# Kernel tuning notes

Measured on AMD Instinct MI355X. Metric: run time of the kernel, lower is better.

## Reference

```python
import jax, jax.numpy as jnp
import numpy as np

B, T, H, S, P, NH, NL = 16, 4096, 1024, 16, 6, 8, 2
EPS = 1e-5

def _ln(x, g, b):
    m = x.mean(-1, keepdims=True)
    v = ((x - m) ** 2).mean(-1, keepdims=True)
    return (x - m) / jnp.sqrt(v + EPS) * g + b

def _mha(q, k, v, in_w, in_b, out_w, out_b, kpm):
    dh = H // NH
    wq, wk, wv = jnp.split(in_w, 3, axis=0)
    bq, bk, bv = jnp.split(in_b, 3, axis=0)
    qh = (q @ wq.T + bq).reshape(q.shape[0], q.shape[1], NH, dh)
    kh = (k @ wk.T + bk).reshape(k.shape[0], k.shape[1], NH, dh)
    vh = (v @ wv.T + bv).reshape(v.shape[0], v.shape[1], NH, dh)
    sc = jnp.einsum('bqhd,bkhd->bhqk', qh, kh) / np.float32(np.sqrt(dh))
    if kpm is not None:
        sc = jnp.where(kpm[:, None, None, :], -1e30, sc)
    a = jax.nn.softmax(sc, axis=-1)
    o = jnp.einsum('bhqk,bkhd->bqhd', a, vh).reshape(q.shape[0], q.shape[1], H)
    return o @ out_w.T + out_b

def _segment_pool(hidden, mask):
    # vectorized ragged per-segment mean over the valid prefix of each sequence
    L = mask.sum(-1)  # [B] valid lengths (assumed >= S)
    s = jnp.arange(S + 1, dtype=jnp.float32)
    bounds = jnp.floor(s[None, :] * L[:, None].astype(jnp.float32) / S).astype(jnp.int32)  # [B,S+1]
    pos = jnp.arange(T)
    valid = pos[None, :] < L[:, None]  # [B,T]
    seg_id = (pos[None, :, None] >= bounds[:, None, 1:S]).sum(-1)  # [B,T] in [0,S-1]
    oh = ((seg_id[:, :, None] == jnp.arange(S)) & valid[:, :, None]).astype(hidden.dtype)  # [B,T,S]
    seg_sum = jnp.einsum('bts,bth->bsh', oh, hidden)
    cnt = oh.sum(1)  # [B,S]
    seg_states = seg_sum / jnp.maximum(cnt, 1.0)[..., None]
    return seg_states, cnt > 0

def setup_inputs() -> dict:
    key = jax.random.key(0)
    ks = jax.random.split(key, 32)
    p = lambda k, shp: (jax.random.normal(k, shp, jnp.float32) * 0.02)
    token_states = jax.random.normal(ks[0], (B, T, H), jnp.float32)
    lengths = jax.random.randint(ks[1], (B,), T // 2, T + 1)
    attention_mask = (jnp.arange(T)[None, :] < lengths[:, None]).astype(jnp.int32)
    inp = dict(
        token_states=token_states, attention_mask=attention_mask,
        sa_in_w=p(ks[2], (3 * H, H)), sa_in_b=jnp.zeros((3 * H,)),
        sa_out_w=p(ks[3], (H, H)), sa_out_b=jnp.zeros((H,)),
        ln_g=jnp.ones((H,)), ln_b=jnp.zeros((H,)),
        sal_w1=p(ks[4], (H, H)), sal_b1=jnp.zeros((H,)),
        sal_w2=p(ks[5], (1, H)), sal_b2=jnp.zeros((1,)),
        plan_q=p(ks[6], (P, H)),
        qa_in_w=p(ks[7], (3 * H, H)), qa_in_b=jnp.zeros((3 * H,)),
        qa_out_w=p(ks[8], (H, H)), qa_out_b=jnp.zeros((H,)),
        r_in_w=p(ks[9], (NL, 3 * H, H)), r_in_b=jnp.zeros((NL, 3 * H)),
        r_out_w=p(ks[10], (NL, H, H)), r_out_b=jnp.zeros((NL, H)),
        r_ln1_g=jnp.ones((NL, H)), r_ln1_b=jnp.zeros((NL, H)),
        r_ln2_g=jnp.ones((NL, H)), r_ln2_b=jnp.zeros((NL, H)),
        r_w1=p(ks[11], (NL, 4 * H, H)), r_b1=jnp.zeros((NL, 4 * H)),
        r_w2=p(ks[12], (NL, H, 4 * H)), r_b2=jnp.zeros((NL, H)),
    )
    return inp

def reference(token_states, attention_mask, sa_in_w, sa_in_b, sa_out_w, sa_out_b,
              ln_g, ln_b, sal_w1, sal_b1, sal_w2, sal_b2, plan_q,
              qa_in_w, qa_in_b, qa_out_w, qa_out_b,
              r_in_w, r_in_b, r_out_w, r_out_b,
              r_ln1_g, r_ln1_b, r_ln2_g, r_ln2_b, r_w1, r_b1, r_w2, r_b2):
    seg, seg_mask = _segment_pool(token_states, attention_mask)
    kpm = ~seg_mask
    attn = _mha(seg, seg, seg, sa_in_w, sa_in_b, sa_out_w, sa_out_b, kpm)
    seg = _ln(seg + attn, ln_g, ln_b)
    h = jax.nn.gelu(seg @ sal_w1.T + sal_b1, approximate=False)
    logits = (h @ sal_w2.T + sal_b2)[..., 0]
    logits = jnp.where(seg_mask, logits, -10000.0)
    sal = jax.nn.softmax(logits, axis=-1)
    wseg = seg * sal[..., None]
    query = jnp.broadcast_to(plan_q[None], (token_states.shape[0], P, H))
    plan = _mha(query, wseg, wseg, qa_in_w, qa_in_b, qa_out_w, qa_out_b, kpm)
    for l in range(NL):  # norm_first TransformerEncoder layers
        y = _ln(plan, r_ln1_g[l], r_ln1_b[l])
        plan = plan + _mha(y, y, y, r_in_w[l], r_in_b[l], r_out_w[l], r_out_b[l], None)
        y = _ln(plan, r_ln2_g[l], r_ln2_b[l])
        y = jax.nn.gelu(y @ r_w1[l].T + r_b1[l], approximate=False) @ r_w2[l].T + r_b2[l]
        plan = plan + y
    entropy = -(sal * jnp.log(sal + 1e-8)).sum(-1).mean()
    nrm = jnp.maximum(jnp.linalg.norm(plan, axis=-1, keepdims=True), 1e-12)
    npn = plan / nrm
    sim = jnp.einsum('bph,bqh->bpq', npn, npn)
    off = sim * (1.0 - jnp.eye(P, dtype=sim.dtype))
    redundancy = (off ** 2).sum() / (plan.shape[0] * P * (P - 1))
    return plan, sal, entropy, redundancy
```

## Files before the change

### kernel.cpp

```cpp
#include <hip/hip_runtime.h>
#include <hip/hip_bf16.h>
#include <math.h>

#define BB 16
#define TT 4096
#define HH 1024
#define SS 16
#define PP 6
#define NHH 8
#define DHH 128
#define NLL 2

typedef __hip_bfloat16 bf16;

__device__ __forceinline__ float b2f(bf16 x){ return __bfloat162float(x); }
__device__ __forceinline__ float us2f(unsigned short u){ return __uint_as_float(((unsigned)u) << 16); }

template<int ISBF>
__device__ __forceinline__ float ldw(const void* p, size_t i){
    if (ISBF) return b2f(((const bf16*)p)[i]);
    else      return ((const float*)p)[i];
}

__global__ void k_len(const int* __restrict__ mask, int* __restrict__ L,
                      const unsigned* __restrict__ lng, float* __restrict__ scal,
                      int* __restrict__ flag){
    int b = blockIdx.x, tid = threadIdx.x;
    if (b == 0 && tid == 0){
        scal[0] = 0.f; scal[1] = 0.f; scal[2] = 0.f; scal[3] = 0.f;
        flag[0] = (lng[0] == 0x3F800000u) ? 0 : 1;
    }
    int s = 0;
    for (int t = tid; t < TT; t += 256) s += mask[b*TT + t];
    __shared__ int red[256];
    red[tid] = s; __syncthreads();
    for (int w = 128; w > 0; w >>= 1){ if (tid < w) red[tid] += red[tid+w]; __syncthreads(); }
    if (tid == 0) L[b] = red[0];
}

template<int ISBF>
__device__ void segpool_body(const void* __restrict__ tok, const int* __restrict__ L,
                             float* __restrict__ seg){
    __shared__ float sm[8*1024];
    int s = blockIdx.x, b = blockIdx.y, tid = threadIdx.x;
    int len = L[b];
    int lo = (s*len)/SS, hi = ((s+1)*len)/SS;
    float inv = 1.0f/(float)(hi-lo);
    if (ISBF){
        int ro = tid >> 7;
        int c8 = (tid & 127) << 3;
        float a[8];
        #pragma unroll
        for (int i = 0; i < 8; ++i) a[i] = 0.f;
        const unsigned short* t = (const unsigned short*)tok;
        for (int tt = lo + ro; tt < hi; tt += 8){
            uint4 u = *(const uint4*)(t + ((size_t)(b*TT + tt))*HH + c8);
            a[0] += us2f((unsigned short)(u.x & 0xffff)); a[1] += us2f((unsigned short)(u.x >> 16));
            a[2] += us2f((unsigned short)(u.y & 0xffff)); a[3] += us2f((unsigned short)(u.y >> 16));
            a[4] += us2f((unsigned short)(u.z & 0xffff)); a[5] += us2f((unsigned short)(u.z >> 16));
            a[6] += us2f((unsigned short)(u.w & 0xffff)); a[7] += us2f((unsigned short)(u.w >> 16));
        }
        #pragma unroll
        for (int i = 0; i < 8; ++i) sm[ro*1024 + c8 + i] = a[i];
        __syncthreads();
        if (ro == 0){
            #pragma unroll
            for (int r = 1; r < 8; ++r)
                #pragma unroll
                for (int i = 0; i < 8; ++i) a[i] += sm[r*1024 + c8 + i];
            float* o = seg + ((size_t)(b*SS + s))*HH + c8;
            #pragma unroll
            for (int i = 0; i < 8; ++i) o[i] = a[i]*inv;
        }
    } else {
        int ro = tid >> 8;
        int c4 = (tid & 255) << 2;
        float a[4] = {0.f,0.f,0.f,0.f};
        const float* t = (const float*)tok;
        for (int tt = lo + ro; tt < hi; tt += 4){
            float4 u = *(const float4*)(t + ((size_t)(b*TT + tt))*HH + c4);
            a[0] += u.x; a[1] += u.y; a[2] += u.z; a[3] += u.w;
        }
        #pragma unroll
        for (int i = 0; i < 4; ++i) sm[ro*1024 + c4 + i] = a[i];
        __syncthreads();
        if (ro == 0){
            #pragma unroll
            for (int r = 1; r < 4; ++r)
                #pragma unroll
                for (int i = 0; i < 4; ++i) a[i] += sm[r*1024 + c4 + i];
            float* o = seg + ((size_t)(b*SS + s))*HH + c4;
            #pragma unroll
            for (int i = 0; i < 4; ++i) o[i] = a[i]*inv;
        }
    }
}
__global__ __launch_bounds__(1024) void k_segpool(const void* __restrict__ tok,
                          const int* __restrict__ L,
                          float* __restrict__ seg, const int* __restrict__ flag){
    if (*flag) segpool_body<1>(tok, L, seg); else segpool_body<0>(tok, L, seg);
}

__global__ __launch_bounds__(256,2) void k_gemmsk(
        const float* __restrict__ X, const void* __restrict__ W,
        float* __restrict__ part, int N, int K, int M,
        size_t offW, int kChunk, const int* __restrict__ flag){
    __shared__ float As[16][68], Bs[16][68];
    const int tid = threadIdx.x;
    const int r0 = blockIdx.y*64, c0 = blockIdx.x*64;
    const int tx = tid & 15, ty = tid >> 4;
    const int sr = tid >> 2;
    const int sk = (tid & 3) << 2;
    const int kbeg = blockIdx.z * kChunk, kend = kbeg + kChunk;
    const int isbf = *flag;
    float c[4][4] = {{0.f,0.f,0.f,0.f},{0.f,0.f,0.f,0.f},{0.f,0.f,0.f,0.f},{0.f,0.f,0.f,0.f}};
    for (int k0 = kbeg; k0 < kend; k0 += 16){
        float4 av = make_float4(0.f,0.f,0.f,0.f);
        if (r0 + sr < N) av = *(const float4*)(X + (size_t)(r0+sr)*K + k0 + sk);
        float4 bv;
        if (isbf){
            ushort4 u = *(const ushort4*)((const bf16*)W + offW + (size_t)(c0+sr)*K + k0 + sk);
            bv = make_float4(us2f(u.x), us2f(u.y), us2f(u.z), us2f(u.w));
        } else {
            bv = *(const float4*)((const float*)W + offW + (size_t)(c0+sr)*K + k0 + sk);
        }
        As[sk+0][sr]=av.x; As[sk+1][sr]=av.y; As[sk+2][sr]=av.z; As[sk+3][sr]=av.w;
        Bs[sk+0][sr]=bv.x; Bs[sk+1][sr]=bv.y; Bs[sk+2][sr]=bv.z; Bs[sk+3][sr]=bv.w;
        __syncthreads();
        #pragma unroll
        for (int kk = 0; kk < 16; ++kk){
            float4 a = *(const float4*)&As[kk][ty<<2];
            float4 b = *(const float4*)&Bs[kk][tx<<2];
            c[0][0] += a.x*b.x; c[0][1] += a.x*b.y; c[0][2] += a.x*b.z; c[0][3] += a.x*b.w;
            c[1][0] += a.y*b.x; c[1][1] += a.y*b.y; c[1][2] += a.y*b.z; c[1][3] += a.y*b.w;
            c[2][0] += a.z*b.x; c[2][1] += a.z*b.y; c[2][2] += a.z*b.z; c[2][3] += a.z*b.w;
            c[3][0] += a.w*b.x; c[3][1] += a.w*b.y; c[3][2] += a.w*b.z; c[3][3] += a.w*b.w;
        }
        __syncthreads();
    }
    float* dst = part + (size_t)blockIdx.z * ((size_t)N * M);
    #pragma unroll
    for (int i = 0; i < 4; ++i){
        int r = r0 + (ty<<2) + i;
        if (r < N){
            float4 st = make_float4(c[i][0], c[i][1], c[i][2], c[i][3]);
            *(float4*)(dst + (size_t)r*M + c0 + (tx<<2)) = st;
        }
    }
}

template<int ACT, int RES>
__global__ void k_epi(const float* __restrict__ part, const void* __restrict__ bias,
                      const float* __restrict__ R, float* __restrict__ Y,
                      int M, int offB, int total, int SK, const int* __restrict__ flag){
    int i = blockIdx.x*256 + threadIdx.x;
    if (i >= total) return;
    float v = 0.f;
    for (int z = 0; z < SK; ++z) v += part[(size_t)z*total + i];
    int col = i % M;
    v += (*flag) ? b2f(((const bf16*)bias)[offB + col]) : ((const float*)bias)[offB + col];
    if (ACT == 1) v = 0.5f*v*(1.0f + erff(v*0.70710678118654752f));
    if (RES == 1) v += R[i];
    Y[i] = v;
}

template<int ISBF, int RES>
__device__ void epiln_body(const float* __restrict__ part, const void* __restrict__ bias,
                           const float* __restrict__ R, float* __restrict__ Y,
                           float* __restrict__ Z, const void* __restrict__ g,
                           const void* __restrict__ bta,
                           int offB, int lnoff, int N, int SK){
    int row = blockIdx.x, tid = threadIdx.x;
    size_t base = (size_t)row*HH;
    size_t total = (size_t)N*HH;
    float v[4]; float s = 0.f, sq = 0.f;
    #pragma unroll
    for (int u = 0; u < 4; ++u){
        int c = tid + u*256;
        float a = 0.f;
        for (int z = 0; z < SK; ++z) a += part[(size_t)z*total + base + c];
        a += ldw<ISBF>(bias, (size_t)(offB + c));
        if (RES) a += R[base + c];
        Y[base + c] = a;
        v[u] = a; s += a; sq += a*a;
    }
    __shared__ float r1[256], r2[256];
    r1[tid] = s; r2[tid] = sq; __syncthreads();
    for (int w = 128; w > 0; w >>= 1){
        if (tid < w){ r1[tid] += r1[tid+w]; r2[tid] += r2[tid+w]; }
        __syncthreads();
    }
    float mean = r1[0]*(1.0f/HH);
    float var  = fmaxf(r2[0]*(1.0f/HH) - mean*mean, 0.f);
    float rstd = rsqrtf(var + 1e-5f);
    #pragma unroll
    for (int u = 0; u < 4; ++u){
        int c = tid + u*256;
        Z[base + c] = (v[u]-mean)*rstd*ldw<ISBF>(g, (size_t)(lnoff+c)) + ldw<ISBF>(bta, (size_t)(lnoff+c));
    }
}
template<int RES>
__global__ void k_epiln(const float* __restrict__ part, const void* __restrict__ bias,
                        const float* __restrict__ R, float* __restrict__ Y,
                        float* __restrict__ Z, const void* __restrict__ g,
                        const void* __restrict__ bta, int offB, int lnoff, int N, int SK,
                        const int* __restrict__ flag){
    if (*flag) epiln_body<1,RES>(part,bias,R,Y,Z,g,bta,offB,lnoff,N,SK);
    else       epiln_body<0,RES>(part,bias,R,Y,Z,g,bta,offB,lnoff,N,SK);
}

static void gemm_sk(hipStream_t st, const float* X, const void* W, const void* bias,
                    const float* R, float* Y, float* part, const int* flag,
                    int N, int K, int M, size_t offW, int offB, int SK, int act, int res){
    dim3 g(M/64, (N+63)/64, SK);
    k_gemmsk<<<g, 256, 0, st>>>(X, W, part, N, K, M, offW, K/SK, flag);
    int total = N*M;
    int nb = (total + 255)/256;
    if (act){
        if (res) k_epi<1,1><<<nb,256,0,st>>>(part, bias, R, Y, M, offB, total, SK, flag);
        else     k_epi<1,0><<<nb,256,0,st>>>(part, bias, R, Y, M, offB, total, SK, flag);
    } else {
        if (res) k_epi<0,1><<<nb,256,0,st>>>(part, bias, R, Y, M, offB, total, SK, flag);
        else     k_epi<0,0><<<nb,256,0,st>>>(part, bias, R, Y, M, offB, total, SK, flag);
    }
}

static void gemm_skln(hipStream_t st, const float* X, const void* W, const void* bias,
                      const float* R, float* Y, float* Z, const void* g, const void* bta,
                      float* part, const int* flag,
                      int N, int K, int M, size_t offW, int offB, int lnoff, int SK, int res){
    dim3 gr(M/64, (N+63)/64, SK);
    k_gemmsk<<<gr, 256, 0, st>>>(X, W, part, N, K, M, offW, K/SK, flag);
    if (res) k_epiln<1><<<N,256,0,st>>>(part, bias, R, Y, Z, g, bta, offB, lnoff, N, SK, flag);
    else     k_epiln<0><<<N,256,0,st>>>(part, bias, R, Y, Z, g, bta, offB, lnoff, N, SK, flag);
}

__global__ void k_attn(const float* __restrict__ Qb, const float* __restrict__ Kb,
                       const float* __restrict__ Vb, float* __restrict__ O,
                       int nq, int nk, int sQ, int sKV, int qShared){
    __shared__ float Qs[16][132], Ks[16][132], Vs[16][132];
    __shared__ float sc[16][17];
    int b = blockIdx.x / NHH, h = blockIdx.x % NHH;
    int tid = threadIdx.x;
    for (int idx = tid; idx < nq*32; idx += 256){
        int i = idx >> 5, d4 = (idx & 31) << 2;
        int r = qShared ? i : (b*nq + i);
        *(float4*)&Qs[i][d4] = *(const float4*)&Qb[(size_t)r*sQ + h*DHH + d4];
    }
    for (int idx = tid; idx < nk*32; idx += 256){
        int j = idx >> 5, d4 = (idx & 31) << 2;
        *(float4*)&Ks[j][d4] = *(const float4*)&Kb[(size_t)(b*nk + j)*sKV + h*DHH + d4];
        *(float4*)&Vs[j][d4] = *(const float4*)&Vb[(size_t)(b*nk + j)*sKV + h*DHH + d4];
    }
    __syncthreads();
    const float scale = 0.0883883476483184406f;
    for (int idx = tid; idx < nq*nk; idx += 256){
        int i = idx / nk, j = idx - i*nk;
        const float4* qp = (const float4*)&Qs[i][0];
        const float4* kp = (const float4*)&Ks[j][0];
        float ax=0.f, ay=0.f, az=0.f, aw=0.f;
        #pragma unroll
        for (int k4 = 0; k4 < 32; ++k4){
            float4 a = qp[k4], c = kp[k4];
            ax += a.x*c.x; ay += a.y*c.y; az += a.z*c.z; aw += a.w*c.w;
        }
        sc[i][j] = (ax+ay+az+aw) * scale;
    }
    __syncthreads();
    if (tid < nq){
        float m = -1e30f;
        for (int j = 0; j < nk; ++j) m = fmaxf(m, sc[tid][j]);
        float ssum = 0.f;
        for (int j = 0; j < nk; ++j){ float e = expf(sc[tid][j] - m); sc[tid][j] = e; ssum += e; }
        float inv = 1.0f/ssum;
        for (int j = 0; j < nk; ++j) sc[tid][j] *= inv;
    }
    __syncthreads();
    for (int idx = tid; idx < nq*32; idx += 256){
        int i = idx >> 5, d4 = (idx & 31) << 2;
        float ox=0.f, oy=0.f, oz=0.f, ow=0.f;
        for (int j = 0; j < nk; ++j){
            float s = sc[i][j];
            float4 v = *(const float4*)&Vs[j][d4];
            ox += s*v.x; oy += s*v.y; oz += s*v.z; ow += s*v.w;
        }
        float4 o = make_float4(ox,oy,oz,ow);
        *(float4*)&O[(size_t)(b*nq + i)*HH + h*DHH + d4] = o;
    }
}

template<int ISBF>
__device__ void sallogit_body(const float* __restrict__ Hbuf, const void* __restrict__ w2,
                              const void* __restrict__ b2v, float* __restrict__ lg){
    int s = blockIdx.x, b = blockIdx.y, tid = threadIdx.x;
    const float* hr = Hbuf + (size_t)(b*SS + s)*HH;
    float acc = 0.f;
    #pragma unroll
    for (int u = 0; u < 4; ++u){ int c = tid + u*256; acc += hr[c]*ldw<ISBF>(w2, (size_t)c); }
    __shared__ float red[256];
    red[tid] = acc; __syncthreads();
    for (int w = 128; w > 0; w >>= 1){ if (tid < w) red[tid] += red[tid+w]; __syncthreads(); }
    if (tid == 0) lg[b*SS + s] = red[0] + ldw<ISBF>(b2v, 0);
}
__global__ void k_sallogit(const float* __restrict__ Hbuf, const void* __restrict__ w2,
                           const void* __restrict__ b2v, float* __restrict__ lg,
                           const int* __restrict__ flag){
    if (*flag) sallogit_body<1>(Hbuf,w2,b2v,lg); else sallogit_body<0>(Hbuf,w2,b2v,lg);
}
__global__ void k_salsm(const float* __restrict__ lg, float* __restrict__ sal,
                        float* __restrict__ scal){
    int b = blockIdx.x;
    if (threadIdx.x == 0){
        float e[SS];
        float m = -1e30f;
        for (int s = 0; s < SS; ++s) m = fmaxf(m, lg[b*SS+s]);
        float ssum = 0.f;
        for (int s = 0; s < SS; ++s){ e[s] = expf(lg[b*SS+s]-m); ssum += e[s]; }
        float inv = 1.0f/ssum, ent = 0.f;
        for (int s = 0; s < SS; ++s){
            float p = e[s]*inv;
            sal[b*SS+s] = p;
            ent -= p*logf(p + 1e-8f);
        }
        atomicAdd(&scal[0], ent);
    }
}

__global__ void k_wseg(const float* __restrict__ seg, const float* __restrict__ sal,
                       float* __restrict__ wseg){
    int i = blockIdx.x*256 + threadIdx.x;
    wseg[i] = seg[i]*sal[i/HH];
}

__global__ void k_cvt(const void* __restrict__ in, float* __restrict__ out, int n,
                      const int* __restrict__ flag){
    int i = blockIdx.x*256 + threadIdx.x;
    if (i < n){
        if (*flag) out[i] = b2f(((const bf16*)in)[i]);
        else       out[i] = ((const float*)in)[i];
    }
}

__device__ const int g_PR[21] = {0,1,2,3,4,5, 0,0,0,0,0,1,1,1,1,2,2,2,3,3,4};
__device__ const int g_QR[21] = {0,1,2,3,4,5, 1,2,3,4,5,2,3,4,5,3,4,5,4,5,5};

__global__ void k_dots(const float* __restrict__ plan, float* __restrict__ dots){
    int t = blockIdx.x % 21, b = blockIdx.x / 21, tid = threadIdx.x;
    const float* X = plan + (size_t)b*PP*HH + (size_t)g_PR[t]*HH;
    const float* Yv = plan + (size_t)b*PP*HH + (size_t)g_QR[t]*HH;
    float acc = 0.f;
    #pragma unroll
    for (int u = 0; u < 4; ++u){ int c = tid + u*256; acc += X[c]*Yv[c]; }
    __shared__ float red[256];
    red[tid] = acc; __syncthreads();
    for (int w = 128; w > 0; w >>= 1){ if (tid < w) red[tid] += red[tid+w]; __syncthreads(); }
    if (tid == 0) dots[b*24 + t] = red[0];
}
__global__ void k_red2(const float* __restrict__ dots, float* __restrict__ scal){
    __shared__ float tot[BB];
    int tid = threadIdx.x;
    if (tid < BB){
        float n[PP];
        #pragma unroll
        for (int p = 0; p < PP; ++p) n[p] = fmaxf(sqrtf(dots[tid*24 + p]), 1e-12f);
        float total = 0.f;
        for (int k = 6; k < 21; ++k){
            float s = dots[tid*24 + k] / (n[g_PR[k]]*n[g_QR[k]]);
            total += 2.0f*s*s;
        }
        tot[tid] = total;
    }
    __syncthreads();
    if (tid == 0){
        float s = 0.f;
        for (int i = 0; i < BB; ++i) s += tot[i];
        scal[1] = s;
    }
}

__global__ void k_out(const float* __restrict__ plan, const float* __restrict__ sal,
                      const float* __restrict__ scal, void* __restrict__ outv,
                      const int* __restrict__ flag){
    int i = blockIdx.x*256 + threadIdx.x;
    const int NPLAN = BB*PP*HH;
    const int NSAL  = BB*SS;
    float v;
    if (i < NPLAN) v = plan[i];
    else if (i < NPLAN + NSAL) v = sal[i - NPLAN];
    else if (i == NPLAN + NSAL) v = scal[0] * (1.0f/BB);
    else if (i == NPLAN + NSAL + 1) v = scal[1] * (1.0f/(BB*PP*(PP-1)));
    else return;
    if (*flag) ((bf16*)outv)[i] = __float2bfloat16(v);
    else       ((float*)outv)[i] = v;
}

extern "C" void kernel_launch(void* const* d_in, const int* in_sizes, int n_in,
                              void* d_out, int out_size, void* d_ws, size_t ws_size,
                              hipStream_t stream) {
    const void* tok      = d_in[0];
    const int*  mask     = (const int*)d_in[1];
    const void* sa_in_w  = d_in[2];
    const void* sa_in_b  = d_in[3];
    const void* sa_out_w = d_in[4];
    const void* sa_out_b = d_in[5];
    const void* ln_g     = d_in[6];
    const void* ln_b     = d_in[7];
    const void* sal_w1   = d_in[8];
    const void* sal_b1   = d_in[9];
    const void* sal_w2   = d_in[10];
    const void* sal_b2   = d_in[11];
    const void* plan_q   = d_in[12];
    const void* qa_in_w  = d_in[13];
    const void* qa_in_b  = d_in[14];
    const void* qa_out_w = d_in[15];
    const void* qa_out_b = d_in[16];
    const void* r_in_w   = d_in[17];
    const void* r_in_b   = d_in[18];
    const void* r_out_w  = d_in[19];
    const void* r_out_b  = d_in[20];
    const void* r_ln1_g  = d_in[21];
    const void* r_ln1_b  = d_in[22];
    const void* r_ln2_g  = d_in[23];
    const void* r_ln2_b  = d_in[24];
    const void* r_w1     = d_in[25];
    const void* r_b1     = d_in[26];
    const void* r_w2     = d_in[27];
    const void* r_b2     = d_in[28];

    float* ws   = (float*)d_ws;
    float* seg  = ws;
    float* qkv  = seg  + BB*SS*HH;
    float* t1   = qkv  + BB*SS*3*HH;
    float* t2   = t1   + BB*SS*HH;
    float* plan = t2   + BB*SS*HH;
    float* ybuf = plan + BB*PP*HH;
    float* qkv2 = ybuf + BB*PP*HH;
    float* pbuf = qkv2 + BB*PP*4*HH;
    float* sal  = pbuf + BB*PP*HH;
    float* qx   = sal  + BB*SS;
    float* qh   = qx   + PP*HH;
    float* lgbuf= qh   + PP*HH;
    float* dots = lgbuf+ BB*SS;
    float* part = dots + BB*24;
    float* scal = part + 4*BB*SS*3*HH;
    int*   Lw   = (int*)(scal + 4);
    int*   flag = Lw + BB;

    k_len<<<BB, 256, 0, stream>>>(mask, Lw, (const unsigned*)ln_g, scal, flag);
    k_segpool<<<dim3(SS, BB), 1024, 0, stream>>>(tok, Lw, seg, flag);

    gemm_sk(stream, seg, sa_in_w, sa_in_b, nullptr, qkv, part, flag,
            BB*SS, HH, 3*HH, (size_t)0, 0, 4, 0, 0);
    k_attn<<<BB*NHH, 256, 0, stream>>>(qkv, qkv+HH, qkv+2*HH, t1, SS, SS, 3*HH, 3*HH, 0);
    gemm_skln(stream, t1, sa_out_w, sa_out_b, seg, t2, seg, ln_g, ln_b, part, flag,
              BB*SS, HH, HH, (size_t)0, 0, 0, 8, 1);

    gemm_sk(stream, seg, sal_w1, sal_b1, nullptr, t1, part, flag,
            BB*SS, HH, HH, (size_t)0, 0, 8, 1, 0);
    k_sallogit<<<dim3(SS, BB), 256, 0, stream>>>(t1, sal_w2, sal_b2, lgbuf, flag);
    k_salsm<<<BB, 64, 0, stream>>>(lgbuf, sal, scal);
    k_wseg<<<BB*SS*HH/256, 256, 0, stream>>>(seg, sal, t2);

    k_cvt<<<(PP*HH+255)/256, 256, 0, stream>>>(plan_q, qx, PP*HH, flag);
    gemm_sk(stream, qx, qa_in_w, qa_in_b, nullptr, qh, part, flag,
            PP, HH, HH, (size_t)0, 0, 16, 0, 0);
    gemm_sk(stream, t2, qa_in_w, qa_in_b, nullptr, qkv, part, flag,
            BB*SS, HH, 2*HH, (size_t)HH*HH, HH, 4, 0, 0);
    k_attn<<<BB*NHH, 256, 0, stream>>>(qh, qkv, qkv+HH, pbuf, PP, SS, HH, 2*HH, 1);
    gemm_skln(stream, pbuf, qa_out_w, qa_out_b, nullptr, plan, ybuf, r_ln1_g, r_ln1_b,
              part, flag, BB*PP, HH, HH, (size_t)0, 0, 0, 8, 0);

    for (int l = 0; l < NLL; ++l){
        gemm_sk(stream, ybuf, r_in_w, r_in_b, nullptr, qkv2, part, flag,
                BB*PP, HH, 3*HH, (size_t)l*3*HH*HH, l*3*HH, 4, 0, 0);
        k_attn<<<BB*NHH, 256, 0, stream>>>(qkv2, qkv2+HH, qkv2+2*HH, pbuf, PP, PP, 3*HH, 3*HH, 0);
        gemm_skln(stream, pbuf, r_out_w, r_out_b, plan, plan, ybuf, r_ln2_g, r_ln2_b,
                  part, flag, BB*PP, HH, HH, (size_t)l*HH*HH, l*HH, l*HH, 8, 1);
        gemm_sk(stream, ybuf, r_w1, r_b1, nullptr, qkv2, part, flag,
                BB*PP, HH, 4*HH, (size_t)l*4*HH*HH, l*4*HH, 4, 1, 0);
        if (l < NLL-1){
            gemm_skln(stream, qkv2, r_w2, r_b2, plan, plan, ybuf, r_ln1_g, r_ln1_b,
                      part, flag, BB*PP, 4*HH, HH, (size_t)l*HH*4*HH, l*HH, (l+1)*HH, 16, 1);
        } else {
            gemm_sk(stream, qkv2, r_w2, r_b2, plan, plan, part, flag,
                    BB*PP, 4*HH, HH, (size_t)l*HH*4*HH, l*HH, 16, 0, 1);
        }
    }

    k_dots<<<BB*21, 256, 0, stream>>>(plan, dots);
    k_red2<<<1, 64, 0, stream>>>(dots, scal);
    k_out<<<(BB*PP*HH + BB*SS + 2 + 255)/256, 256, 0, stream>>>(plan, sal, scal, d_out, flag);
}
```

Measured before the change: 882.2 us.

## Use bf16 MFMA GEMM with hi/lo split activations for bf16 weights

Replaces the scalar FP32 LDS-tiled GEMM with a matrix-core path (16x16x32 bf16 MFMA) whenever the weights are bf16. Each activation is split into a bf16 high part and a bf16 residual so that FP32 activation precision is roughly kept. Producer kernels (segpool, epilogues, attention, wseg, cvt) now also write these hi/lo bf16 copies. Split-K factors are retuned as well. The cost is extra memory writes and two MFMAs per K step, plus loading weights directly from global memory with no LDS reuse across waves. The FP32-weight path keeps the old scalar GEMM and only gains the extra conversion stores.

```diff
diff --git a/kernel.cpp b/kernel.cpp
--- a/kernel.cpp
+++ b/kernel.cpp
@@ -12,9 +12,23 @@
 #define NLL 2
 
 typedef __hip_bfloat16 bf16;
+typedef __attribute__((ext_vector_type(8))) short s8v;
+typedef __attribute__((ext_vector_type(4))) float f32x4;
+
+#define MFMA_B16(a,b,c) __builtin_amdgcn_mfma_f32_16x16x32_bf16((a),(b),(c),0,0,0)
 
 __device__ __forceinline__ float b2f(bf16 x){ return __bfloat162float(x); }
 __device__ __forceinline__ float us2f(unsigned short u){ return __uint_as_float(((unsigned)u) << 16); }
+
+__device__ __forceinline__ void split_bf(float x, ushort& h, ushort& l){
+    unsigned xb = __float_as_uint(x);
+    unsigned hh = (xb + 0x7FFFu + ((xb >> 16) & 1u)) >> 16;
+    float hf = __uint_as_float(hh << 16);
+    float r  = x - hf;
+    unsigned rb = __float_as_uint(r);
+    unsigned ll = (rb + 0x7FFFu + ((rb >> 16) & 1u)) >> 16;
+    h = (ushort)hh; l = (ushort)ll;
+}
 
 template<int ISBF>
 __device__ __forceinline__ float ldw(const void* p, size_t i){
@@ -40,7 +54,8 @@
 
 template<int ISBF>
 __device__ void segpool_body(const void* __restrict__ tok, const int* __restrict__ L,
-                             float* __restrict__ seg){
+                             float* __restrict__ seg, ushort* __restrict__ sh,
+                             ushort* __restrict__ sl){
     __shared__ float sm[8*1024];
     int s = blockIdx.x, b = blockIdx.y, tid = threadIdx.x;
     int len = L[b];
@@ -68,9 +83,14 @@
             for (int r = 1; r < 8; ++r)
                 #pragma unroll
                 for (int i = 0; i < 8; ++i) a[i] += sm[r*1024 + c8 + i];
-            float* o = seg + ((size_t)(b*SS + s))*HH + c8;
+            size_t base = ((size_t)(b*SS + s))*HH + c8;
             #pragma unroll
-            for (int i = 0; i < 8; ++i) o[i] = a[i]*inv;
+            for (int i = 0; i < 8; ++i){
+                float v = a[i]*inv;
+                seg[base + i] = v;
+                ushort h, l2; split_bf(v, h, l2);
+                sh[base + i] = h; sl[base + i] = l2;
+            }
         }
     } else {
         int ro = tid >> 8;
@@ -89,69 +109,110 @@
             for (int r = 1; r < 4; ++r)
                 #pragma unroll
                 for (int i = 0; i < 4; ++i) a[i] += sm[r*1024 + c4 + i];
-            float* o = seg + ((size_t)(b*SS + s))*HH + c4;
+            size_t base = ((size_t)(b*SS + s))*HH + c4;
             #pragma unroll
-            for (int i = 0; i < 4; ++i) o[i] = a[i]*inv;
+            for (int i = 0; i < 4; ++i){
+                float v = a[i]*inv;
+                seg[base + i] = v;
+                ushort h, l2; split_bf(v, h, l2);
+                sh[base + i] = h; sl[base + i] = l2;
+            }
         }
     }
 }
 __global__ __launch_bounds__(1024) void k_segpool(const void* __restrict__ tok,
-                          const int* __restrict__ L,
-                          float* __restrict__ seg, const int* __restrict__ flag){
-    if (*flag) segpool_body<1>(tok, L, seg); else segpool_body<0>(tok, L, seg);
-}
-
-__global__ __launch_bounds__(256,2) void k_gemmsk(
-        const float* __restrict__ X, const void* __restrict__ W,
-        float* __restrict__ part, int N, int K, int M,
-        size_t offW, int kChunk, const int* __restrict__ flag){
+                          const int* __restrict__ L, float* __restrict__ seg,
+                          ushort* __restrict__ sh, ushort* __restrict__ sl,
+                          const int* __restrict__ flag){
+    if (*flag) segpool_body<1>(tok, L, seg, sh, sl); else segpool_body<0>(tok, L, seg, sh, sl);
+}
+
+__global__ __launch_bounds__(256,2) void k_gemm_uni(
+        const float* __restrict__ Xf, const ushort* __restrict__ Ah, const ushort* __restrict__ Al,
+        const void* __restrict__ W, float* __restrict__ part,
+        int N, int K, int M, size_t offW, int kChunk, const int* __restrict__ flag){
     __shared__ float As[16][68], Bs[16][68];
     const int tid = threadIdx.x;
-    const int r0 = blockIdx.y*64, c0 = blockIdx.x*64;
-    const int tx = tid & 15, ty = tid >> 4;
-    const int sr = tid >> 2;
-    const int sk = (tid & 3) << 2;
-    const int kbeg = blockIdx.z * kChunk, kend = kbeg + kChunk;
+    const int c0 = blockIdx.x*64;
+    const int kbeg = blockIdx.z * kChunk;
     const int isbf = *flag;
-    float c[4][4] = {{0.f,0.f,0.f,0.f},{0.f,0.f,0.f,0.f},{0.f,0.f,0.f,0.f},{0.f,0.f,0.f,0.f}};
-    for (int k0 = kbeg; k0 < kend; k0 += 16){
-        float4 av = make_float4(0.f,0.f,0.f,0.f);
-        if (r0 + sr < N) av = *(const float4*)(X + (size_t)(r0+sr)*K + k0 + sk);
-        float4 bv;
-        if (isbf){
-            ushort4 u = *(const ushort4*)((const bf16*)W + offW + (size_t)(c0+sr)*K + k0 + sk);
-            bv = make_float4(us2f(u.x), us2f(u.y), us2f(u.z), us2f(u.w));
-        } else {
-            bv = *(const float4*)((const float*)W + offW + (size_t)(c0+sr)*K + k0 + sk);
-        }
-        As[sk+0][sr]=av.x; As[sk+1][sr]=av.y; As[sk+2][sr]=av.z; As[sk+3][sr]=av.w;
-        Bs[sk+0][sr]=bv.x; Bs[sk+1][sr]=bv.y; Bs[sk+2][sr]=bv.z; Bs[sk+3][sr]=bv.w;
-        __syncthreads();
-        #pragma unroll
-        for (int kk = 0; kk < 16; ++kk){
-            float4 a = *(const float4*)&As[kk][ty<<2];
-            float4 b = *(const float4*)&Bs[kk][tx<<2];
-            c[0][0] += a.x*b.x; c[0][1] += a.x*b.y; c[0][2] += a.x*b.z; c[0][3] += a.x*b.w;
-            c[1][0] += a.y*b.x; c[1][1] += a.y*b.y; c[1][2] += a.y*b.z; c[1][3] += a.y*b.w;
-            c[2][0] += a.z*b.x; c[2][1] += a.z*b.y; c[2][2] += a.z*b.z; c[2][3] += a.z*b.w;
-            c[3][0] += a.w*b.x; c[3][1] += a.w*b.y; c[3][2] += a.w*b.z; c[3][3] += a.w*b.w;
-        }
-        __syncthreads();
-    }
-    float* dst = part + (size_t)blockIdx.z * ((size_t)N * M);
-    #pragma unroll
-    for (int i = 0; i < 4; ++i){
-        int r = r0 + (ty<<2) + i;
-        if (r < N){
-            float4 st = make_float4(c[i][0], c[i][1], c[i][2], c[i][3]);
-            *(float4*)(dst + (size_t)r*M + c0 + (tx<<2)) = st;
+    if (isbf){
+        const int l  = tid & 63;
+        const int wv = tid >> 6;
+        const int lr = l & 15;
+        const int lk = (l >> 4) << 3;
+        const int r0 = blockIdx.y*64 + wv*16;
+        const ushort* pah = Ah + (size_t)(r0+lr)*K + lk + kbeg;
+        const ushort* pal = Al + (size_t)(r0+lr)*K + lk + kbeg;
+        const ushort* pw  = (const ushort*)W + offW + (size_t)(c0+lr)*K + lk + kbeg;
+        const size_t w16 = (size_t)16*K;
+        f32x4 a0 = {0.f,0.f,0.f,0.f}, a1 = {0.f,0.f,0.f,0.f};
+        f32x4 a2 = {0.f,0.f,0.f,0.f}, a3 = {0.f,0.f,0.f,0.f};
+        for (int k = 0; k < kChunk; k += 32){
+            s8v ah  = *(const s8v*)pah;
+            s8v alo = *(const s8v*)pal;
+            s8v b0 = *(const s8v*)(pw);
+            s8v b1 = *(const s8v*)(pw + w16);
+            s8v b2 = *(const s8v*)(pw + 2*w16);
+            s8v b3 = *(const s8v*)(pw + 3*w16);
+            a0 = MFMA_B16(ah, b0, a0); a1 = MFMA_B16(ah, b1, a1);
+            a2 = MFMA_B16(ah, b2, a2); a3 = MFMA_B16(ah, b3, a3);
+            a0 = MFMA_B16(alo, b0, a0); a1 = MFMA_B16(alo, b1, a1);
+            a2 = MFMA_B16(alo, b2, a2); a3 = MFMA_B16(alo, b3, a3);
+            pah += 32; pal += 32; pw += 32;
+        }
+        float* dst = part + (size_t)blockIdx.z * ((size_t)N * M);
+        const int rb = r0 + ((l>>4)<<2);
+        #pragma unroll
+        for (int rg = 0; rg < 4; ++rg){
+            int r = rb + rg;
+            if (r < N){
+                float* dr = dst + (size_t)r*M + c0 + lr;
+                dr[0]  = a0[rg];
+                dr[16] = a1[rg];
+                dr[32] = a2[rg];
+                dr[48] = a3[rg];
+            }
+        }
+    } else {
+        const int r0 = blockIdx.y*64;
+        const int tx = tid & 15, ty = tid >> 4;
+        const int sr = tid >> 2;
+        const int sk = (tid & 3) << 2;
+        float c[4][4] = {{0.f,0.f,0.f,0.f},{0.f,0.f,0.f,0.f},{0.f,0.f,0.f,0.f},{0.f,0.f,0.f,0.f}};
+        for (int k0 = kbeg; k0 < kbeg + kChunk; k0 += 16){
+            float4 av = make_float4(0.f,0.f,0.f,0.f);
+            if (r0 + sr < N) av = *(const float4*)(Xf + (size_t)(r0+sr)*K + k0 + sk);
+            float4 bv = *(const float4*)((const float*)W + offW + (size_t)(c0+sr)*K + k0 + sk);
+            As[sk+0][sr]=av.x; As[sk+1][sr]=av.y; As[sk+2][sr]=av.z; As[sk+3][sr]=av.w;
+            Bs[sk+0][sr]=bv.x; Bs[sk+1][sr]=bv.y; Bs[sk+2][sr]=bv.z; Bs[sk+3][sr]=bv.w;
+            __syncthreads();
+            #pragma unroll
+            for (int kk = 0; kk < 16; ++kk){
+                float4 a = *(const float4*)&As[kk][ty<<2];
+                float4 b = *(const float4*)&Bs[kk][tx<<2];
+                c[0][0] += a.x*b.x; c[0][1] += a.x*b.y; c[0][2] += a.x*b.z; c[0][3] += a.x*b.w;
+                c[1][0] += a.y*b.x; c[1][1] += a.y*b.y; c[1][2] += a.y*b.z; c[1][3] += a.y*b.w;
+                c[2][0] += a.z*b.x; c[2][1] += a.z*b.y; c[2][2] += a.z*b.z; c[2][3] += a.z*b.w;
+                c[3][0] += a.w*b.x; c[3][1] += a.w*b.y; c[3][2] += a.w*b.z; c[3][3] += a.w*b.w;
+            }
+            __syncthreads();
+        }
+        float* dst = part + (size_t)blockIdx.z * ((size_t)N * M);
+        #pragma unroll
+        for (int i = 0; i < 4; ++i){
+            int r = r0 + (ty<<2) + i;
+            if (r < N){
+                float4 st = make_float4(c[i][0], c[i][1], c[i][2], c[i][3]);
+                *(float4*)(dst + (size_t)r*M + c0 + (tx<<2)) = st;
+            }
         }
     }
 }
 
 template<int ACT, int RES>
 __global__ void k_epi(const float* __restrict__ part, const void* __restrict__ bias,
-                      const float* __restrict__ R, float* __restrict__ Y,
+                      const float* R, float* Y, ushort* Yh, ushort* Yl,
                       int M, int offB, int total, int SK, const int* __restrict__ flag){
     int i = blockIdx.x*256 + threadIdx.x;
     if (i >= total) return;
@@ -162,13 +223,14 @@
     if (ACT == 1) v = 0.5f*v*(1.0f + erff(v*0.70710678118654752f));
     if (RES == 1) v += R[i];
     Y[i] = v;
+    if (Yh){ ushort h, l; split_bf(v, h, l); Yh[i] = h; Yl[i] = l; }
 }
 
 template<int ISBF, int RES>
 __device__ void epiln_body(const float* __restrict__ part, const void* __restrict__ bias,
-                           const float* __restrict__ R, float* __restrict__ Y,
-                           float* __restrict__ Z, const void* __restrict__ g,
-                           const void* __restrict__ bta,
+                           const float* R, float* Y, float* Z,
+                           ushort* __restrict__ Zh, ushort* __restrict__ Zl,
+                           const void* __restrict__ g, const void* __restrict__ bta,
                            int offB, int lnoff, int N, int SK){
     int row = blockIdx.x, tid = threadIdx.x;
     size_t base = (size_t)row*HH;
@@ -196,47 +258,53 @@
     #pragma unroll
     for (int u = 0; u < 4; ++u){
         int c = tid + u*256;
-        Z[base + c] = (v[u]-mean)*rstd*ldw<ISBF>(g, (size_t)(lnoff+c)) + ldw<ISBF>(bta, (size_t)(lnoff+c));
+        float zv = (v[u]-mean)*rstd*ldw<ISBF>(g, (size_t)(lnoff+c)) + ldw<ISBF>(bta, (size_t)(lnoff+c));
+        Z[base + c] = zv;
+        ushort h, l; split_bf(zv, h, l);
+        Zh[base + c] = h; Zl[base + c] = l;
     }
 }
 template<int RES>
 __global__ void k_epiln(const float* __restrict__ part, const void* __restrict__ bias,
-                        const float* __restrict__ R, float* __restrict__ Y,
-                        float* __restrict__ Z, const void* __restrict__ g,
-                        const void* __restrict__ bta, int offB, int lnoff, int N, int SK,
-                        const int* __restrict__ flag){
-    if (*flag) epiln_body<1,RES>(part,bias,R,Y,Z,g,bta,offB,lnoff,N,SK);
-    else       epiln_body<0,RES>(part,bias,R,Y,Z,g,bta,offB,lnoff,N,SK);
-}
-
-static void gemm_sk(hipStream_t st, const float* X, const void* W, const void* bias,
-                    const float* R, float* Y, float* part, const int* flag,
-                    int N, int K, int M, size_t offW, int offB, int SK, int act, int res){
+                        const float* R, float* Y, float* Z,
+                        ushort* __restrict__ Zh, ushort* __restrict__ Zl,
+                        const void* __restrict__ g, const void* __restrict__ bta,
+                        int offB, int lnoff, int N, int SK, const int* __restrict__ flag){
+    if (*flag) epiln_body<1,RES>(part,bias,R,Y,Z,Zh,Zl,g,bta,offB,lnoff,N,SK);
+    else       epiln_body<0,RES>(part,bias,R,Y,Z,Zh,Zl,g,bta,offB,lnoff,N,SK);
+}
+
+static void gemm2(hipStream_t st, const float* Xf, const ushort* Ah, const ushort* Al,
+                  const void* W, const void* bias, const float* R, float* Y,
+                  ushort* Yh, ushort* Yl, float* part, const int* flag,
+                  int N, int K, int M, size_t offW, int offB, int SK, int act, int res){
     dim3 g(M/64, (N+63)/64, SK);
-    k_gemmsk<<<g, 256, 0, st>>>(X, W, part, N, K, M, offW, K/SK, flag);
+    k_gemm_uni<<<g, 256, 0, st>>>(Xf, Ah, Al, W, part, N, K, M, offW, K/SK, flag);
     int total = N*M;
     int nb = (total + 255)/256;
     if (act){
-        if (res) k_epi<1,1><<<nb,256,0,st>>>(part, bias, R, Y, M, offB, total, SK, flag);
-        else     k_epi<1,0><<<nb,256,0,st>>>(part, bias, R, Y, M, offB, total, SK, flag);
+        if (res) k_epi<1,1><<<nb,256,0,st>>>(part, bias, R, Y, Yh, Yl, M, offB, total, SK, flag);
+        else     k_epi<1,0><<<nb,256,0,st>>>(part, bias, R, Y, Yh, Yl, M, offB, total, SK, flag);
     } else {
-        if (res) k_epi<0,1><<<nb,256,0,st>>>(part, bias, R, Y, M, offB, total, SK, flag);
-        else     k_epi<0,0><<<nb,256,0,st>>>(part, bias, R, Y, M, offB, total, SK, flag);
-    }
-}
-
-static void gemm_skln(hipStream_t st, const float* X, const void* W, const void* bias,
-                      const float* R, float* Y, float* Z, const void* g, const void* bta,
-                      float* part, const int* flag,
-                      int N, int K, int M, size_t offW, int offB, int lnoff, int SK, int res){
+        if (res) k_epi<0,1><<<nb,256,0,st>>>(part, bias, R, Y, Yh, Yl, M, offB, total, SK, flag);
+        else     k_epi<0,0><<<nb,256,0,st>>>(part, bias, R, Y, Yh, Yl, M, offB, total, SK, flag);
+    }
+}
+
+static void gemm2ln(hipStream_t st, const float* Xf, const ushort* Ah, const ushort* Al,
+                    const void* W, const void* bias, const float* R, float* Y,
+                    float* Z, ushort* Zh, ushort* Zl, const void* g, const void* bta,
+                    float* part, const int* flag,
+                    int N, int K, int M, size_t offW, int offB, int lnoff, int SK, int res){
     dim3 gr(M/64, (N+63)/64, SK);
-    k_gemmsk<<<gr, 256, 0, st>>>(X, W, part, N, K, M, offW, K/SK, flag);
-    if (res) k_epiln<1><<<N,256,0,st>>>(part, bias, R, Y, Z, g, bta, offB, lnoff, N, SK, flag);
-    else     k_epiln<0><<<N,256,0,st>>>(part, bias, R, Y, Z, g, bta, offB, lnoff, N, SK, flag);
+    k_gemm_uni<<<gr, 256, 0, st>>>(Xf, Ah, Al, W, part, N, K, M, offW, K/SK, flag);
+    if (res) k_epiln<1><<<N,256,0,st>>>(part, bias, R, Y, Z, Zh, Zl, g, bta, offB, lnoff, N, SK, flag);
+    else     k_epiln<0><<<N,256,0,st>>>(part, bias, R, Y, Z, Zh, Zl, g, bta, offB, lnoff, N, SK, flag);
 }
 
 __global__ void k_attn(const float* __restrict__ Qb, const float* __restrict__ Kb,
                        const float* __restrict__ Vb, float* __restrict__ O,
+                       ushort* __restrict__ Oh, ushort* __restrict__ Ol,
                        int nq, int nk, int sQ, int sKV, int qShared){
     __shared__ float Qs[16][132], Ks[16][132], Vs[16][132];
     __shared__ float sc[16][17];
@@ -284,8 +352,14 @@
             float4 v = *(const float4*)&Vs[j][d4];
             ox += s*v.x; oy += s*v.y; oz += s*v.z; ow += s*v.w;
         }
-        float4 o = make_float4(ox,oy,oz,ow);
-        *(float4*)&O[(size_t)(b*nq + i)*HH + h*DHH + d4] = o;
+        size_t oidx = (size_t)(b*nq + i)*HH + h*DHH + d4;
+        *(float4*)&O[oidx] = make_float4(ox,oy,oz,ow);
+        if (Oh){
+            ushort4 hv, lv;
+            split_bf(ox, hv.x, lv.x); split_bf(oy, hv.y, lv.y);
+            split_bf(oz, hv.z, lv.z); split_bf(ow, hv.w, lv.w);
+            *(ushort4*)&Oh[oidx] = hv; *(ushort4*)&Ol[oidx] = lv;
+        }
     }
 }
 
@@ -327,18 +401,25 @@
 }
 
 __global__ void k_wseg(const float* __restrict__ seg, const float* __restrict__ sal,
-                       float* __restrict__ wseg){
+                       float* __restrict__ wseg, ushort* __restrict__ wh,
+                       ushort* __restrict__ wl){
     int i = blockIdx.x*256 + threadIdx.x;
-    wseg[i] = seg[i]*sal[i/HH];
-}
-
-__global__ void k_cvt(const void* __restrict__ in, float* __restrict__ out, int n,
-                      const int* __restrict__ flag){
+    float v = seg[i]*sal[i/HH];
+    wseg[i] = v;
+    ushort h, l; split_bf(v, h, l);
+    wh[i] = h; wl[i] = l;
+}
+
+__global__ void k_cvt(const void* __restrict__ in, float* __restrict__ out,
+                      ushort* __restrict__ oh, ushort* __restrict__ ol,
+                      int n, int ntot, const int* __restrict__ flag){
     int i = blockIdx.x*256 + threadIdx.x;
-    if (i < n){
-        if (*flag) out[i] = b2f(((const bf16*)in)[i]);
-        else       out[i] = ((const float*)in)[i];
-    }
+    if (i >= ntot) return;
+    float v = 0.f;
+    if (i < n) v = (*flag) ? b2f(((const bf16*)in)[i]) : ((const float*)in)[i];
+    out[i] = v;
+    ushort h, l; split_bf(v, h, l);
+    oh[i] = h; ol[i] = l;
 }
 
 __device__ const int g_PR[21] = {0,1,2,3,4,5, 0,0,0,0,0,1,1,1,1,2,2,2,3,3,4};
@@ -438,52 +519,66 @@
     float* pbuf = qkv2 + BB*PP*4*HH;
     float* sal  = pbuf + BB*PP*HH;
     float* qx   = sal  + BB*SS;
-    float* qh   = qx   + PP*HH;
+    float* qh   = qx   + 16*HH;
     float* lgbuf= qh   + PP*HH;
     float* dots = lgbuf+ BB*SS;
     float* part = dots + BB*24;
-    float* scal = part + 4*BB*SS*3*HH;
+    ushort* segh = (ushort*)(part + 4*BB*SS*3*HH);
+    ushort* segl = segh + BB*SS*HH;
+    ushort* t1h  = segl + BB*SS*HH;
+    ushort* t1l  = t1h  + BB*SS*HH;
+    ushort* t2h  = t1l  + BB*SS*HH;
+    ushort* t2l  = t2h  + BB*SS*HH;
+    ushort* pbh  = t2l  + BB*SS*HH;
+    ushort* pbl  = pbh  + BB*PP*HH;
+    ushort* ybh  = pbl  + BB*PP*HH;
+    ushort* ybl  = ybh  + BB*PP*HH;
+    ushort* ffh  = ybl  + BB*PP*HH;
+    ushort* ffl  = ffh  + BB*PP*4*HH;
+    ushort* qxh  = ffl  + BB*PP*4*HH;
+    ushort* qxl  = qxh  + 16*HH;
+    float* scal = (float*)(qxl + 16*HH);
     int*   Lw   = (int*)(scal + 4);
     int*   flag = Lw + BB;
 
     k_len<<<BB, 256, 0, stream>>>(mask, Lw, (const unsigned*)ln_g, scal, flag);
-    k_segpool<<<dim3(SS, BB), 1024, 0, stream>>>(tok, Lw, seg, flag);
-
-    gemm_sk(stream, seg, sa_in_w, sa_in_b, nullptr, qkv, part, flag,
-            BB*SS, HH, 3*HH, (size_t)0, 0, 4, 0, 0);
-    k_attn<<<BB*NHH, 256, 0, stream>>>(qkv, qkv+HH, qkv+2*HH, t1, SS, SS, 3*HH, 3*HH, 0);
-    gemm_skln(stream, t1, sa_out_w, sa_out_b, seg, t2, seg, ln_g, ln_b, part, flag,
-              BB*SS, HH, HH, (size_t)0, 0, 0, 8, 1);
-
-    gemm_sk(stream, seg, sal_w1, sal_b1, nullptr, t1, part, flag,
-            BB*SS, HH, HH, (size_t)0, 0, 8, 1, 0);
+    k_segpool<<<dim3(SS, BB), 1024, 0, stream>>>(tok, Lw, seg, segh, segl, flag);
+
+    gemm2(stream, seg, segh, segl, sa_in_w, sa_in_b, nullptr, qkv, nullptr, nullptr,
+          part, flag, BB*SS, HH, 3*HH, (size_t)0, 0, 2, 0, 0);
+    k_attn<<<BB*NHH, 256, 0, stream>>>(qkv, qkv+HH, qkv+2*HH, t1, t1h, t1l, SS, SS, 3*HH, 3*HH, 0);
+    gemm2ln(stream, t1, t1h, t1l, sa_out_w, sa_out_b, seg, t2, seg, segh, segl, ln_g, ln_b,
+            part, flag, BB*SS, HH, HH, (size_t)0, 0, 0, 4, 1);
+
+    gemm2(stream, seg, segh, segl, sal_w1, sal_b1, nullptr, t1, nullptr, nullptr,
+          part, flag, BB*SS, HH, HH, (size_t)0, 0, 4, 1, 0);
     k_sallogit<<<dim3(SS, BB), 256, 0, stream>>>(t1, sal_w2, sal_b2, lgbuf, flag);
     k_salsm<<<BB, 64, 0, stream>>>(lgbuf, sal, scal);
-    k_wseg<<<BB*SS*HH/256, 256, 0, stream>>>(seg, sal, t2);
-
-    k_cvt<<<(PP*HH+255)/256, 256, 0, stream>>>(plan_q, qx, PP*HH, flag);
-    gemm_sk(stream, qx, qa_in_w, qa_in_b, nullptr, qh, part, flag,
-            PP, HH, HH, (size_t)0, 0, 16, 0, 0);
-    gemm_sk(stream, t2, qa_in_w, qa_in_b, nullptr, qkv, part, flag,
-            BB*SS, HH, 2*HH, (size_t)HH*HH, HH, 4, 0, 0);
-    k_attn<<<BB*NHH, 256, 0, stream>>>(qh, qkv, qkv+HH, pbuf, PP, SS, HH, 2*HH, 1);
-    gemm_skln(stream, pbuf, qa_out_w, qa_out_b, nullptr, plan, ybuf, r_ln1_g, r_ln1_b,
-              part, flag, BB*PP, HH, HH, (size_t)0, 0, 0, 8, 0);
+    k_wseg<<<BB*SS*HH/256, 256, 0, stream>>>(seg, sal, t2, t2h, t2l);
+
+    k_cvt<<<(16*HH)/256, 256, 0, stream>>>(plan_q, qx, qxh, qxl, PP*HH, 16*HH, flag);
+    gemm2(stream, qx, qxh, qxl, qa_in_w, qa_in_b, nullptr, qh, nullptr, nullptr,
+          part, flag, PP, HH, HH, (size_t)0, 0, 8, 0, 0);
+    gemm2(stream, t2, t2h, t2l, qa_in_w, qa_in_b, nullptr, qkv, nullptr, nullptr,
+          part, flag, BB*SS, HH, 2*HH, (size_t)HH*HH, HH, 2, 0, 0);
+    k_attn<<<BB*NHH, 256, 0, stream>>>(qh, qkv, qkv+HH, pbuf, pbh, pbl, PP, SS, HH, 2*HH, 1);
+    gemm2ln(stream, pbuf, pbh, pbl, qa_out_w, qa_out_b, nullptr, plan, ybuf, ybh, ybl,
+            r_ln1_g, r_ln1_b, part, flag, BB*PP, HH, HH, (size_t)0, 0, 0, 8, 0);
 
     for (int l = 0; l < NLL; ++l){
-        gemm_sk(stream, ybuf, r_in_w, r_in_b, nullptr, qkv2, part, flag,
-                BB*PP, HH, 3*HH, (size_t)l*3*HH*HH, l*3*HH, 4, 0, 0);
-        k_attn<<<BB*NHH, 256, 0, stream>>>(qkv2, qkv2+HH, qkv2+2*HH, pbuf, PP, PP, 3*HH, 3*HH, 0);
-        gemm_skln(stream, pbuf, r_out_w, r_out_b, plan, plan, ybuf, r_ln2_g, r_ln2_b,
-                  part, flag, BB*PP, HH, HH, (size_t)l*HH*HH, l*HH, l*HH, 8, 1);
-        gemm_sk(stream, ybuf, r_w1, r_b1, nullptr, qkv2, part, flag,
-                BB*PP, HH, 4*HH, (size_t)l*4*HH*HH, l*4*HH, 4, 1, 0);
+        gemm2(stream, ybuf, ybh, ybl, r_in_w, r_in_b, nullptr, qkv2, nullptr, nullptr,
+              part, flag, BB*PP, HH, 3*HH, (size_t)l*3*HH*HH, l*3*HH, 4, 0, 0);
+        k_attn<<<BB*NHH, 256, 0, stream>>>(qkv2, qkv2+HH, qkv2+2*HH, pbuf, pbh, pbl, PP, PP, 3*HH, 3*HH, 0);
+        gemm2ln(stream, pbuf, pbh, pbl, r_out_w, r_out_b, plan, plan, ybuf, ybh, ybl,
+                r_ln2_g, r_ln2_b, part, flag, BB*PP, HH, HH, (size_t)l*HH*HH, l*HH, l*HH, 8, 1);
+        gemm2(stream, ybuf, ybh, ybl, r_w1, r_b1, nullptr, qkv2, ffh, ffl,
+              part, flag, BB*PP, HH, 4*HH, (size_t)l*4*HH*HH, l*4*HH, 2, 1, 0);
         if (l < NLL-1){
-            gemm_skln(stream, qkv2, r_w2, r_b2, plan, plan, ybuf, r_ln1_g, r_ln1_b,
-                      part, flag, BB*PP, 4*HH, HH, (size_t)l*HH*4*HH, l*HH, (l+1)*HH, 16, 1);
+            gemm2ln(stream, qkv2, ffh, ffl, r_w2, r_b2, plan, plan, ybuf, ybh, ybl,
+                    r_ln1_g, r_ln1_b, part, flag, BB*PP, 4*HH, HH, (size_t)l*HH*4*HH, l*HH, (l+1)*HH, 8, 1);
         } else {
-            gemm_sk(stream, qkv2, r_w2, r_b2, plan, plan, part, flag,
-                    BB*PP, 4*HH, HH, (size_t)l*HH*4*HH, l*HH, 16, 0, 1);
+            gemm2(stream, qkv2, ffh, ffl, r_w2, r_b2, plan, plan, nullptr, nullptr,
+                  part, flag, BB*PP, 4*HH, HH, (size_t)l*HH*4*HH, l*HH, 8, 0, 1);
         }
     }
 
```

Result: slower. 951.1 us (+7.8%).
